# Kernel optimization log

Measured on AMD Instinct MI355X. Metric: run time of the kernel, lower is better.

## Reference

```python
import jax, jax.numpy as jnp
import numpy as np

NUM_HEADS = 16
GROUP_NUM = 4
HIDDEN = 1024
HEAD_DIM = HIDDEN // NUM_HEADS
EPS = 1e-5


def layernorm(x, g, b):
    mu = jnp.mean(x, axis=-1, keepdims=True)
    var = jnp.var(x, axis=-1, keepdims=True)
    return (x - mu) * jax.lax.rsqrt(var + EPS) * g + b


def setup_inputs() -> dict:
    key = jax.random.key(0)
    ks = jax.random.split(key, 12)
    s = 0.02
    return {
        "hidden_state": jax.random.normal(ks[0], (2, 2048, HIDDEN), jnp.float32),
        "wq": jax.random.normal(ks[1], (HIDDEN, HIDDEN), jnp.float32) * s,
        "bq": jnp.zeros((HIDDEN,), jnp.float32),
        "wk": jax.random.normal(ks[2], (GROUP_NUM * HEAD_DIM, HIDDEN), jnp.float32) * s,
        "bk": jnp.zeros((GROUP_NUM * HEAD_DIM,), jnp.float32),
        "wv": jax.random.normal(ks[3], (GROUP_NUM * HEAD_DIM, HIDDEN), jnp.float32) * s,
        "bv": jnp.zeros((GROUP_NUM * HEAD_DIM,), jnp.float32),
        "wo": jax.random.normal(ks[4], (HIDDEN, HIDDEN), jnp.float32) * s,
        "bo": jnp.zeros((HIDDEN,), jnp.float32),
        "ln_g": jnp.ones((HIDDEN,), jnp.float32),
        "ln_b": jnp.zeros((HIDDEN,), jnp.float32),
        "w1": jax.random.normal(ks[5], (HIDDEN, HIDDEN), jnp.float32) * s,
        "b1": jnp.zeros((HIDDEN,), jnp.float32),
        "w2": jax.random.normal(ks[6], (HIDDEN, HIDDEN), jnp.float32) * s,
        "b2": jnp.zeros((HIDDEN,), jnp.float32),
        "fln_g": jnp.ones((HIDDEN,), jnp.float32),
        "fln_b": jnp.zeros((HIDDEN,), jnp.float32),
    }


def reference(hidden_state, wq, bq, wk, bk, wv, bv, wo, bo, ln_g, ln_b,
              w1, b1, w2, b2, fln_g, fln_b):
    B, S, H = hidden_state.shape
    hpg = NUM_HEADS // GROUP_NUM  # heads per KV group

    q = hidden_state @ wq.T + bq  # [B,S,H]
    k = hidden_state @ wk.T + bk  # [B,S,G*D]
    v = hidden_state @ wv.T + bv

    q = q.reshape(B, S, NUM_HEADS, HEAD_DIM).transpose(0, 2, 1, 3)      # [B,Hh,S,D]
    k = k.reshape(B, S, GROUP_NUM, HEAD_DIM).transpose(0, 2, 1, 3)      # [B,G,S,D]
    v = v.reshape(B, S, GROUP_NUM, HEAD_DIM).transpose(0, 2, 1, 3)
    # expand KV groups to full head count (consecutive repeat, matching torch expand+reshape)
    k = jnp.repeat(k, hpg, axis=1)  # [B,Hh,S,D]
    v = jnp.repeat(v, hpg, axis=1)

    scale = 1.0 / jnp.sqrt(jnp.float32(HEAD_DIM))
    scores = jnp.einsum('bhsd,bhtd->bhst', q, k) * scale  # [B,Hh,S,S]
    probs = jax.nn.softmax(scores, axis=-1)
    attn = jnp.einsum('bhst,bhtd->bhsd', probs, v)  # [B,Hh,S,D]

    # Faithful to source: transpose(-1,-2) then raw flat view to [B, S, Hh*D]
    attn = jnp.swapaxes(attn, -1, -2).reshape(B, -1, HEAD_DIM * NUM_HEADS)

    out = layernorm(hidden_state + attn @ wo.T + bo, ln_g, ln_b)
    ffn = out @ w1.T + b1
    ffn = jax.nn.relu(ffn) @ w2.T + b2
    return layernorm(out + ffn, fln_g, fln_b)
```

## Files before the change

kernel.cpp:

```cpp
#include <hip/hip_runtime.h>
#include <math.h>

#define HIDDEN 1024
#define SEQ 2048

typedef __attribute__((ext_vector_type(8))) short short8;
typedef __attribute__((ext_vector_type(4))) float f32x4;

__device__ __forceinline__ unsigned short f2bf(float x) {
  union { float f; unsigned u; } c; c.f = x;
  unsigned r = c.u + 0x7FFFu + ((c.u >> 16) & 1u);
  return (unsigned short)(r >> 16);
}
__device__ __forceinline__ float bf2f(unsigned short h) {
  union { unsigned u; float f; } c; c.u = ((unsigned)h) << 16;
  return c.f;
}

__device__ __forceinline__ float fexp2(float x) {
  float r; asm("v_exp_f32 %0, %1" : "=v"(r) : "v"(x)); return r;
}

__device__ __forceinline__ unsigned cvt_pk_bf16(float lo, float hi) {
  unsigned r;
  asm("v_cvt_pk_bf16_f32 %0, %1, %2" : "=v"(r) : "v"(lo), "v"(hi));
  return r;
}

__device__ __forceinline__ void async_copy16(const void* g, void* l) {
  __builtin_amdgcn_global_load_lds(
      (const __attribute__((address_space(1))) unsigned int*)g,
      (__attribute__((address_space(3))) unsigned int*)l, 16, 0, 0);
}

__global__ __launch_bounds__(256) void cvt_all(
    const float* __restrict__ hs, const float* __restrict__ wq,
    const float* __restrict__ wk, const float* __restrict__ wv,
    const float* __restrict__ wo, const float* __restrict__ w1,
    const float* __restrict__ w2,
    unsigned short* __restrict__ hsb, unsigned short* __restrict__ wqb,
    unsigned short* __restrict__ wkb, unsigned short* __restrict__ wvb,
    unsigned short* __restrict__ wob, unsigned short* __restrict__ w1b,
    unsigned short* __restrict__ w2b)
{
  const int i = blockIdx.x * 256 + threadIdx.x;
  const float* src; unsigned short* dst; int off;
  if (i < 1048576)      { src = hs; dst = hsb; off = i; }
  else if (i < 1310720) { src = wq; dst = wqb; off = i - 1048576; }
  else if (i < 1376256) { src = wk; dst = wkb; off = i - 1310720; }
  else if (i < 1441792) { src = wv; dst = wvb; off = i - 1376256; }
  else if (i < 1703936) { src = wo; dst = wob; off = i - 1441792; }
  else if (i < 1966080) { src = w1; dst = w1b; off = i - 1703936; }
  else                  { src = w2; dst = w2b; off = i - 1966080; }
  float4 v = ((const float4*)src)[off];
  ushort4 o;
  o.x = f2bf(v.x); o.y = f2bf(v.y); o.z = f2bf(v.z); o.w = f2bf(v.w);
  ((ushort4*)dst)[off] = o;
}

template<bool RELU>
__global__ __launch_bounds__(256) void gemm_mfma(
    const unsigned short* __restrict__ A, const unsigned short* __restrict__ W,
    const float* __restrict__ bias, unsigned short* __restrict__ C,
    int M, int N, int K)
{
  __shared__ unsigned short As[64 * 64];
  __shared__ unsigned short Bs[64 * 64];
  const int tid = threadIdx.x;
  const int lane = tid & 63, wave = tid >> 6;
  const int ln = lane & 15, quad = lane >> 4;
  const int wm = (wave >> 1) * 32, wn = (wave & 1) * 32;

  const int flat = blockIdx.x;
  const int swz = (flat & 7) * ((int)gridDim.x >> 3) + (flat >> 3);
  const int ntx = N >> 6;
  const int m0 = (swz / ntx) * 64, n0 = (swz % ntx) * 64;

  f32x4 acc[2][2];
#pragma unroll
  for (int i = 0; i < 2; ++i)
#pragma unroll
    for (int j = 0; j < 2; ++j) acc[i][j] = (f32x4){0.f, 0.f, 0.f, 0.f};

  for (int k0 = 0; k0 < K; k0 += 64) {
#pragma unroll
    for (int it = 0; it < 2; ++it) {
      const int c = (wave * 2 + it) * 64 + lane;
      const int row = c >> 3, gc = (c & 7) ^ (row & 7);
      async_copy16(A + (size_t)(m0 + row) * K + k0 + gc * 8,
                   &As[(wave * 2 + it) * 512]);
      async_copy16(W + (size_t)(n0 + row) * K + k0 + gc * 8,
                   &Bs[(wave * 2 + it) * 512]);
    }
    __syncthreads();

    short8 af[2][2], bfr[2][2];
#pragma unroll
    for (int i = 0; i < 2; ++i) {
      const int row = wm + i * 16 + ln;
#pragma unroll
      for (int f = 0; f < 2; ++f) {
        const int ch = row * 8 + ((f * 4 + quad) ^ (row & 7));
        af[i][f] = *(const short8*)&As[ch * 8];
      }
    }
#pragma unroll
    for (int j = 0; j < 2; ++j) {
      const int row = wn + j * 16 + ln;
#pragma unroll
      for (int f = 0; f < 2; ++f) {
        const int ch = row * 8 + ((f * 4 + quad) ^ (row & 7));
        bfr[j][f] = *(const short8*)&Bs[ch * 8];
      }
    }
#pragma unroll
    for (int i = 0; i < 2; ++i)
#pragma unroll
      for (int j = 0; j < 2; ++j) {
        acc[i][j] = __builtin_amdgcn_mfma_f32_16x16x32_bf16(af[i][0], bfr[j][0], acc[i][j], 0, 0, 0);
        acc[i][j] = __builtin_amdgcn_mfma_f32_16x16x32_bf16(af[i][1], bfr[j][1], acc[i][j], 0, 0, 0);
      }
    __syncthreads();
  }

#pragma unroll
  for (int j = 0; j < 2; ++j) {
    const int n = n0 + wn + j * 16 + ln;
    const float bv = bias[n];
#pragma unroll
    for (int i = 0; i < 2; ++i) {
#pragma unroll
      for (int rr = 0; rr < 4; ++rr) {
        const int m = m0 + wm + i * 16 + quad * 4 + rr;
        float v = acc[i][j][rr] + bv;
        if (RELU) v = fmaxf(v, 0.f);
        C[(size_t)m * N + n] = f2bf(v);
      }
    }
  }
}

__global__ __launch_bounds__(256) void gemm_qkv(
    const unsigned short* __restrict__ A,
    const unsigned short* __restrict__ Wq, const unsigned short* __restrict__ Wk,
    const unsigned short* __restrict__ Wv,
    const float* __restrict__ bq, const float* __restrict__ bk,
    const float* __restrict__ bv,
    unsigned short* __restrict__ Qo, unsigned short* __restrict__ Ko,
    unsigned short* __restrict__ Vt)
{
  __shared__ unsigned short As[64 * 64];
  __shared__ unsigned short Bs[128 * 64];

  const int flat = blockIdx.x;
  const int swz = (flat & 7) * 96 + (flat >> 3);
  const int bx = swz % 12, by = swz / 12;

  int mode, nw0;
  const unsigned short* W;
  const float* bias;
  if (bx < 8)       { mode = 0; W = Wq; bias = bq; nw0 = bx * 128; }
  else if (bx < 10) { mode = 1; W = Wk; bias = bk; nw0 = (bx - 8) * 128; }
  else              { mode = 2; W = Wv; bias = bv; nw0 = (bx - 10) * 128; }

  const int tid = threadIdx.x;
  const int lane = tid & 63, wave = tid >> 6;
  const int ln = lane & 15, quad = lane >> 4;
  const int wm = (wave >> 1) * 32, wn = (wave & 1) * 64;
  const int m0 = by * 64;
  const int K = 1024;

  f32x4 acc[2][4];
#pragma unroll
  for (int i = 0; i < 2; ++i)
#pragma unroll
    for (int j = 0; j < 4; ++j) acc[i][j] = (f32x4){0.f, 0.f, 0.f, 0.f};

  for (int k0 = 0; k0 < K; k0 += 64) {
#pragma unroll
    for (int it = 0; it < 2; ++it) {
      const int c = (wave * 2 + it) * 64 + lane;
      const int row = c >> 3, gc = (c & 7) ^ (row & 7);
      async_copy16(A + (size_t)(m0 + row) * K + k0 + gc * 8,
                   &As[(wave * 2 + it) * 512]);
    }
#pragma unroll
    for (int it = 0; it < 4; ++it) {
      const int c = (wave * 4 + it) * 64 + lane;
      const int row = c >> 3, gc = (c & 7) ^ (row & 7);
      async_copy16(W + (size_t)(nw0 + row) * K + k0 + gc * 8,
                   &Bs[(wave * 4 + it) * 512]);
    }
    __syncthreads();

    short8 af[2][2], bfr[4][2];
#pragma unroll
    for (int i = 0; i < 2; ++i) {
      const int row = wm + i * 16 + ln;
#pragma unroll
      for (int f = 0; f < 2; ++f) {
        const int ch = row * 8 + ((f * 4 + quad) ^ (row & 7));
        af[i][f] = *(const short8*)&As[ch * 8];
      }
    }
#pragma unroll
    for (int j = 0; j < 4; ++j) {
      const int row = wn + j * 16 + ln;
#pragma unroll
      for (int f = 0; f < 2; ++f) {
        const int ch = row * 8 + ((f * 4 + quad) ^ (row & 7));
        bfr[j][f] = *(const short8*)&Bs[ch * 8];
      }
    }
#pragma unroll
    for (int i = 0; i < 2; ++i)
#pragma unroll
      for (int j = 0; j < 4; ++j) {
        acc[i][j] = __builtin_amdgcn_mfma_f32_16x16x32_bf16(af[i][0], bfr[j][0], acc[i][j], 0, 0, 0);
        acc[i][j] = __builtin_amdgcn_mfma_f32_16x16x32_bf16(af[i][1], bfr[j][1], acc[i][j], 0, 0, 0);
      }
    __syncthreads();
  }

#pragma unroll
  for (int j = 0; j < 4; ++j) {
    const int nl = nw0 + wn + j * 16 + ln;
    const float bvv = bias[nl];
#pragma unroll
    for (int i = 0; i < 2; ++i) {
#pragma unroll
      for (int rr = 0; rr < 4; ++rr) {
        const int m = m0 + wm + i * 16 + quad * 4 + rr;
        const float v = acc[i][j][rr] + bvv;
        if (mode == 0) {
          Qo[(size_t)m * 1024 + nl] = f2bf(v);
        } else if (mode == 1) {
          Ko[(size_t)m * 256 + nl] = f2bf(v);
        } else {
          const int b = m >> 11, s = m & 2047;
          Vt[((size_t)b * 256 + nl) * SEQ + s] = f2bf(v);
        }
      }
    }
  }
}

__global__ __launch_bounds__(256) void attn_mfma(
    const unsigned short* __restrict__ Q, const unsigned short* __restrict__ Kb,
    const unsigned short* __restrict__ Vt, unsigned short* __restrict__ O)
{
  __shared__ unsigned short Ks[2][64 * 64];
  __shared__ unsigned short Vs[2][64 * 64];

  const int hwb = blockIdx.x;
  const int swz = (hwb & 7) * 32 + (hwb >> 3);
  const int qblk = swz & 7, h = (swz >> 3) & 15, b = swz >> 7, g = h >> 2;

  const int tid = threadIdx.x, lane = tid & 63, wave = tid >> 6;
  const int ln = lane & 15, quad = lane >> 4, q8 = quad * 8;
  const int s0 = qblk * 256;
  const float qscale = 0.125f * 1.44269504f;

  const int ln7 = ln & 7;
  const int x0 = (quad ^ ln7) * 8;
  const int x1 = ((4 + quad) ^ ln7) * 8;

  short8 ones;
#pragma unroll
  for (int e = 0; e < 8; ++e) ones[e] = (short)0x3F80;

  short8 qf[4][2];
#pragma unroll
  for (int qg = 0; qg < 4; ++qg) {
    const unsigned short* qsrc =
        Q + ((size_t)(b * SEQ + s0 + wave * 64 + qg * 16 + ln)) * 1024 + h * 64 + q8;
    qf[qg][0] = *(const short8*)qsrc;
    qf[qg][1] = *(const short8*)(qsrc + 32);
#pragma unroll
    for (int e = 0; e < 8; ++e) {
      qf[qg][0][e] = (short)f2bf(bf2f((unsigned short)qf[qg][0][e]) * qscale);
      qf[qg][1][e] = (short)f2bf(bf2f((unsigned short)qf[qg][1][e]) * qscale);
    }
  }

  const int srow = lane >> 3;
  const int sgcc = (lane & 7) ^ srow;

  auto stage = [&](int t0, int p) {
#pragma unroll
    for (int it = 0; it < 2; ++it) {
      const int row = wave * 16 + it * 8 + srow;
      const int skey = (row & 32) | ((row & 8) << 1) | ((row & 4) << 1) |
                       ((row & 16) >> 2) | (row & 3);
      async_copy16(Kb + (size_t)(b * SEQ + t0 + skey) * 256 + g * 64 + sgcc * 8,
                   &Ks[p][(wave * 2 + it) * 512]);
      async_copy16(Vt + (size_t)(b * 256 + g * 64 + row) * SEQ + t0 + sgcc * 8,
                   &Vs[p][(wave * 2 + it) * 512]);
    }
  };

  f32x4 of[4][4];
  f32x4 ls[4];
#pragma unroll
  for (int qg = 0; qg < 4; ++qg) {
    ls[qg] = (f32x4){0.f, 0.f, 0.f, 0.f};
#pragma unroll
    for (int jd = 0; jd < 4; ++jd) of[qg][jd] = (f32x4){0.f, 0.f, 0.f, 0.f};
  }

  stage(0, 0);

  for (int t = 0; t < 32; ++t) {
    const int p = t & 1;
    if (t < 31) {
      stage((t + 1) * 64, p ^ 1);
      asm volatile("s_waitcnt vmcnt(4)" ::: "memory");
    } else {
      asm volatile("s_waitcnt vmcnt(0)" ::: "memory");
    }
    __builtin_amdgcn_s_barrier();
    asm volatile("" ::: "memory");

    f32x4 sc[4][4];
#pragma unroll
    for (int jn = 0; jn < 4; ++jn) {
      const int krow = (jn * 16 + ln) * 64;
      const short8 kf0 = *(const short8*)&Ks[p][krow + x0];
      const short8 kf1 = *(const short8*)&Ks[p][krow + x1];
#pragma unroll
      for (int qg = 0; qg < 4; ++qg) {
        f32x4 z = (f32x4){0.f, 0.f, 0.f, 0.f};
        z = __builtin_amdgcn_mfma_f32_16x16x32_bf16(kf0, qf[qg][0], z, 0, 0, 0);
        z = __builtin_amdgcn_mfma_f32_16x16x32_bf16(kf1, qf[qg][1], z, 0, 0, 0);
        sc[qg][jn] = z;
      }
    }

    short8 pf[4][2];
#pragma unroll
    for (int qg = 0; qg < 4; ++qg) {
#pragma unroll
      for (int jn = 0; jn < 4; ++jn)
#pragma unroll
        for (int r = 0; r < 4; ++r) sc[qg][jn][r] = fexp2(sc[qg][jn][r]);
#pragma unroll
      for (int F = 0; F < 2; ++F) {
        union { unsigned u[4]; short8 s; } pk;
        pk.u[0] = cvt_pk_bf16(sc[qg][2 * F][0], sc[qg][2 * F][1]);
        pk.u[1] = cvt_pk_bf16(sc[qg][2 * F][2], sc[qg][2 * F][3]);
        pk.u[2] = cvt_pk_bf16(sc[qg][2 * F + 1][0], sc[qg][2 * F + 1][1]);
        pk.u[3] = cvt_pk_bf16(sc[qg][2 * F + 1][2], sc[qg][2 * F + 1][3]);
        pf[qg][F] = pk.s;
      }
      ls[qg] = __builtin_amdgcn_mfma_f32_16x16x32_bf16(pf[qg][0], ones, ls[qg], 0, 0, 0);
      ls[qg] = __builtin_amdgcn_mfma_f32_16x16x32_bf16(pf[qg][1], ones, ls[qg], 0, 0, 0);
    }

#pragma unroll
    for (int jd = 0; jd < 4; ++jd) {
      const int vrow = (jd * 16 + ln) * 64;
      const short8 vf0 = *(const short8*)&Vs[p][vrow + x0];
      const short8 vf1 = *(const short8*)&Vs[p][vrow + x1];
#pragma unroll
      for (int qg = 0; qg < 4; ++qg) {
        of[qg][jd] = __builtin_amdgcn_mfma_f32_16x16x32_bf16(pf[qg][0], vf0, of[qg][jd], 0, 0, 0);
        of[qg][jd] = __builtin_amdgcn_mfma_f32_16x16x32_bf16(pf[qg][1], vf1, of[qg][jd], 0, 0, 0);
      }
    }

    asm volatile("" ::: "memory");
    __builtin_amdgcn_s_barrier();
    asm volatile("" ::: "memory");
  }

#pragma unroll
  for (int qg = 0; qg < 4; ++qg) {
    float inv[4];
#pragma unroll
    for (int r = 0; r < 4; ++r) inv[r] = 1.0f / ls[qg][r];
    const int sbase = s0 + wave * 64 + qg * 16 + quad * 4;
#pragma unroll
    for (int jd = 0; jd < 4; ++jd) {
      const int d = jd * 16 + ln;
      ushort4 ov;
      ov.x = f2bf(of[qg][jd][0] * inv[0]);
      ov.y = f2bf(of[qg][jd][1] * inv[1]);
      ov.z = f2bf(of[qg][jd][2] * inv[2]);
      ov.w = f2bf(of[qg][jd][3] * inv[3]);
      *(ushort4*)&O[((size_t)b * 1024 + h * 64 + d) * SEQ + sbase] = ov;
    }
  }
}

__device__ __forceinline__ void ln_core(float x[4], const float* gam, const float* bet,
                                        int tid, float out[4]) {
  float s1 = x[0] + x[1] + x[2] + x[3];
  float s2 = x[0] * x[0] + x[1] * x[1] + x[2] * x[2] + x[3] * x[3];
#pragma unroll
  for (int off = 1; off < 64; off <<= 1) {
    s1 += __shfl_xor(s1, off);
    s2 += __shfl_xor(s2, off);
  }
  __shared__ float r1[4], r2[4];
  const int wave = tid >> 6;
  if ((tid & 63) == 0) { r1[wave] = s1; r2[wave] = s2; }
  __syncthreads();
  s1 = r1[0] + r1[1] + r1[2] + r1[3];
  s2 = r2[0] + r2[1] + r2[2] + r2[3];
  const float mu  = s1 * (1.0f / HIDDEN);
  const float var = s2 * (1.0f / HIDDEN) - mu * mu;
  const float inv = rsqrtf(var + 1e-5f);
  float4 gv = *(const float4*)&gam[tid * 4];
  float4 bv = *(const float4*)&bet[tid * 4];
  out[0] = (x[0] - mu) * inv * gv.x + bv.x;
  out[1] = (x[1] - mu) * inv * gv.y + bv.y;
  out[2] = (x[2] - mu) * inv * gv.z + bv.z;
  out[3] = (x[3] - mu) * inv * gv.w + bv.w;
}

__global__ __launch_bounds__(256) void resid_ln1(
    const float* __restrict__ X, const unsigned short* __restrict__ Y,
    const float* __restrict__ gam, const float* __restrict__ bet,
    unsigned short* __restrict__ outb)
{
  const int row = blockIdx.x, tid = threadIdx.x;
  const size_t base = (size_t)row * HIDDEN + tid * 4;
  float4 a = *(const float4*)&X[base];
  ushort4 yv = *(const ushort4*)&Y[base];
  float x[4] = {a.x + bf2f(yv.x), a.y + bf2f(yv.y), a.z + bf2f(yv.z), a.w + bf2f(yv.w)};
  float o[4];
  ln_core(x, gam, bet, tid, o);
  ushort4 ov;
  ov.x = f2bf(o[0]); ov.y = f2bf(o[1]); ov.z = f2bf(o[2]); ov.w = f2bf(o[3]);
  *(ushort4*)&outb[base] = ov;
}

__global__ __launch_bounds__(256) void resid_ln2(
    const unsigned short* __restrict__ X, const unsigned short* __restrict__ Y,
    const float* __restrict__ gam, const float* __restrict__ bet,
    float* __restrict__ out)
{
  const int row = blockIdx.x, tid = threadIdx.x;
  const size_t base = (size_t)row * HIDDEN + tid * 4;
  ushort4 xv = *(const ushort4*)&X[base];
  ushort4 yv = *(const ushort4*)&Y[base];
  float x[4] = {bf2f(xv.x) + bf2f(yv.x), bf2f(xv.y) + bf2f(yv.y),
                bf2f(xv.z) + bf2f(yv.z), bf2f(xv.w) + bf2f(yv.w)};
  float o[4];
  ln_core(x, gam, bet, tid, o);
  float4 ov; ov.x = o[0]; ov.y = o[1]; ov.z = o[2]; ov.w = o[3];
  *(float4*)&out[base] = ov;
}

extern "C" void kernel_launch(void* const* d_in, const int* in_sizes, int n_in,
                              void* d_out, int out_size, void* d_ws, size_t ws_size,
                              hipStream_t stream)
{
  (void)in_sizes; (void)n_in; (void)out_size; (void)ws_size;
  const float* hs  = (const float*)d_in[0];
  const float* wq  = (const float*)d_in[1];
  const float* bq  = (const float*)d_in[2];
  const float* wk  = (const float*)d_in[3];
  const float* bk  = (const float*)d_in[4];
  const float* wv  = (const float*)d_in[5];
  const float* bvp = (const float*)d_in[6];
  const float* wo  = (const float*)d_in[7];
  const float* bo  = (const float*)d_in[8];
  const float* lng = (const float*)d_in[9];
  const float* lnb = (const float*)d_in[10];
  const float* w1  = (const float*)d_in[11];
  const float* b1  = (const float*)d_in[12];
  const float* w2  = (const float*)d_in[13];
  const float* b2  = (const float*)d_in[14];
  const float* flg = (const float*)d_in[15];
  const float* flb = (const float*)d_in[16];
  float* out = (float*)d_out;

  unsigned short* w = (unsigned short*)d_ws;
  unsigned short* wqb = w;
  unsigned short* wkb = w + 1048576;
  unsigned short* wvb = w + 1310720;
  unsigned short* wob = w + 1572864;
  unsigned short* w1b = w + 2621440;
  unsigned short* w2b = w + 3670016;
  unsigned short* hsb = w + 4718592;
  unsigned short* qb  = w + 8912896;
  unsigned short* kb  = w + 13107200;
  unsigned short* vt  = w + 14155776;
  unsigned short* att = w + 15204352;
  unsigned short* f1b = hsb;
  unsigned short* yb  = qb;
  unsigned short* obb = att;
  unsigned short* f2b = qb;

  dim3 blk(256);
  cvt_all<<<dim3(8704), blk, 0, stream>>>(hs, wq, wk, wv, wo, w1, w2,
                                          hsb, wqb, wkb, wvb, wob, w1b, w2b);

  gemm_qkv<<<dim3(768), blk, 0, stream>>>(hsb, wqb, wkb, wvb, bq, bk, bvp,
                                          qb, kb, vt);
  attn_mfma<<<dim3(256), blk, 0, stream>>>(qb, kb, vt, att);
  gemm_mfma<false><<<dim3(1024), blk, 0, stream>>>(att, wob, bo, yb, 4096, 1024, 1024);
  resid_ln1<<<dim3(4096), blk, 0, stream>>>(hs, yb, lng, lnb, obb);
  gemm_mfma<true><<<dim3(1024), blk, 0, stream>>>(obb, w1b, b1, f1b, 4096, 1024, 1024);
  gemm_mfma<false><<<dim3(1024), blk, 0, stream>>>(f1b, w2b, b2, f2b, 4096, 1024, 1024);
  resid_ln2<<<dim3(4096), blk, 0, stream>>>(obb, f2b, flg, flb, out);
}
```

Measured before the change: 244.1 us.

## Split attention KV loop across two blocks and combine with a reduce kernel

The attention kernel's key/value loop is split into two halves, doubling the grid from 256 to 512 blocks. Each block writes unnormalized bf16 numerators and fp32 row sums. A new attn_reduce kernel then adds the two partials and divides by the combined sum. This aims to fill the GPU's CUs more fully during attention. In exchange it adds an extra launch, extra global traffic, and bf16 rounding of the unnormalized partials, and it reuses the hsb and wqb buffers as scratch.

```diff
diff --git a/kernel.cpp b/kernel.cpp
--- a/kernel.cpp
+++ b/kernel.cpp
@@ -247,14 +247,20 @@
 
 __global__ __launch_bounds__(256) void attn_mfma(
     const unsigned short* __restrict__ Q, const unsigned short* __restrict__ Kb,
-    const unsigned short* __restrict__ Vt, unsigned short* __restrict__ O)
+    const unsigned short* __restrict__ Vt,
+    unsigned short* __restrict__ N0, unsigned short* __restrict__ N1,
+    float* __restrict__ LS)
 {
   __shared__ unsigned short Ks[2][64 * 64];
   __shared__ unsigned short Vs[2][64 * 64];
 
   const int hwb = blockIdx.x;
-  const int swz = (hwb & 7) * 32 + (hwb >> 3);
-  const int qblk = swz & 7, h = (swz >> 3) & 15, b = swz >> 7, g = h >> 2;
+  const int swz = (hwb & 7) * 64 + (hwb >> 3);
+  const int qblk = swz & 7, half = (swz >> 3) & 1, h = (swz >> 4) & 15, b = swz >> 8;
+  const int g = h >> 2;
+
+  unsigned short* __restrict__ numO = half ? N1 : N0;
+  float* __restrict__ lsO = LS + half * 65536;
 
   const int tid = threadIdx.x, lane = tid & 63, wave = tid >> 6;
   const int ln = lane & 15, quad = lane >> 4, q8 = quad * 8;
@@ -308,12 +314,13 @@
     for (int jd = 0; jd < 4; ++jd) of[qg][jd] = (f32x4){0.f, 0.f, 0.f, 0.f};
   }
 
-  stage(0, 0);
-
-  for (int t = 0; t < 32; ++t) {
-    const int p = t & 1;
-    if (t < 31) {
-      stage((t + 1) * 64, p ^ 1);
+  const int tbase = half * 16;
+  stage(tbase * 64, 0);
+
+  for (int tt = 0; tt < 16; ++tt) {
+    const int p = tt & 1;
+    if (tt < 15) {
+      stage((tbase + tt + 1) * 64, p ^ 1);
       asm volatile("s_waitcnt vmcnt(4)" ::: "memory");
     } else {
       asm volatile("s_waitcnt vmcnt(0)" ::: "memory");
@@ -375,21 +382,43 @@
 
 #pragma unroll
   for (int qg = 0; qg < 4; ++qg) {
-    float inv[4];
-#pragma unroll
-    for (int r = 0; r < 4; ++r) inv[r] = 1.0f / ls[qg][r];
     const int sbase = s0 + wave * 64 + qg * 16 + quad * 4;
+    if (ln == 0) {
+#pragma unroll
+      for (int r = 0; r < 4; ++r)
+        lsO[(b * 16 + h) * 2048 + sbase + r] = ls[qg][r];
+    }
 #pragma unroll
     for (int jd = 0; jd < 4; ++jd) {
       const int d = jd * 16 + ln;
       ushort4 ov;
-      ov.x = f2bf(of[qg][jd][0] * inv[0]);
-      ov.y = f2bf(of[qg][jd][1] * inv[1]);
-      ov.z = f2bf(of[qg][jd][2] * inv[2]);
-      ov.w = f2bf(of[qg][jd][3] * inv[3]);
-      *(ushort4*)&O[((size_t)b * 1024 + h * 64 + d) * SEQ + sbase] = ov;
-    }
-  }
+      ov.x = f2bf(of[qg][jd][0]);
+      ov.y = f2bf(of[qg][jd][1]);
+      ov.z = f2bf(of[qg][jd][2]);
+      ov.w = f2bf(of[qg][jd][3]);
+      *(ushort4*)&numO[((size_t)b * 1024 + h * 64 + d) * SEQ + sbase] = ov;
+    }
+  }
+}
+
+__global__ __launch_bounds__(256) void attn_reduce(
+    const unsigned short* __restrict__ N0, unsigned short* att,
+    const float* __restrict__ LS)
+{
+  const int i = (blockIdx.x * 256 + threadIdx.x) * 4;
+  const int row = i >> 11, s = i & 2047;
+  const int h = (row >> 6) & 15, b = row >> 10;
+  const int lsi = (b * 16 + h) * 2048 + s;
+  const float4 l0 = *(const float4*)&LS[lsi];
+  const float4 l1 = *(const float4*)&LS[65536 + lsi];
+  const ushort4 a = *(const ushort4*)&N0[i];
+  const ushort4 c = *(const ushort4*)&att[i];
+  ushort4 o;
+  o.x = f2bf((bf2f(a.x) + bf2f(c.x)) / (l0.x + l1.x));
+  o.y = f2bf((bf2f(a.y) + bf2f(c.y)) / (l0.y + l1.y));
+  o.z = f2bf((bf2f(a.z) + bf2f(c.z)) / (l0.z + l1.z));
+  o.w = f2bf((bf2f(a.w) + bf2f(c.w)) / (l0.w + l1.w));
+  *(ushort4*)&att[i] = o;
 }
 
 __device__ __forceinline__ void ln_core(float x[4], const float* gam, const float* bet,
@@ -492,6 +521,7 @@
   unsigned short* yb  = qb;
   unsigned short* obb = att;
   unsigned short* f2b = qb;
+  float* lsbuf = (float*)wqb;
 
   dim3 blk(256);
   cvt_all<<<dim3(8704), blk, 0, stream>>>(hs, wq, wk, wv, wo, w1, w2,
@@ -499,7 +529,8 @@
 
   gemm_qkv<<<dim3(768), blk, 0, stream>>>(hsb, wqb, wkb, wvb, bq, bk, bvp,
                                           qb, kb, vt);
-  attn_mfma<<<dim3(256), blk, 0, stream>>>(qb, kb, vt, att);
+  attn_mfma<<<dim3(512), blk, 0, stream>>>(qb, kb, vt, hsb, att, lsbuf);
+  attn_reduce<<<dim3(4096), blk, 0, stream>>>(hsb, att, lsbuf);
   gemm_mfma<false><<<dim3(1024), blk, 0, stream>>>(att, wob, bo, yb, 4096, 1024, 1024);
   resid_ln1<<<dim3(4096), blk, 0, stream>>>(hs, yb, lng, lnb, obb);
   gemm_mfma<true><<<dim3(1024), blk, 0, stream>>>(obb, w1b, b1, f1b, 4096, 1024, 1024);
```

Measured after the change: 246.7 us. Within noise of the previous version (+1.1%).
